# Performance work log

Hardware: AMD Instinct MI355X
Metric: run time of the kernel (lower is better)

Reference implementation:

```python
import jax, jax.numpy as jnp
import numpy as np

OMEGA = 0.3        # self.omega
NU = 0.2           # self.nu
LAMBDA_DECAY = 0.1 # lambda_decay
MU_INIT = 0.25     # nn.Parameter init
EPS_DENOM = 1e-8
EPS_SQRT = 1e-24   # safe sqrt (avoids nan grad at exactly-zero distance)


def setup_inputs() -> dict:
    key = jax.random.key(0)
    k1, k2, k3, k4 = jax.random.split(key, 4)
    T, D = 4096, 896  # seq_len, Qwen2.5-0.5B hidden size
    return {
        "hidden_states": jax.random.normal(k1, (T, D), dtype=jnp.float32),
        "m_t": jax.random.uniform(k2, (T,), dtype=jnp.float32),
        "c_t": jax.random.uniform(k3, (T,), dtype=jnp.float32),
        "d_t": jax.random.uniform(k4, (T,), dtype=jnp.float32),
        "mu": jnp.asarray(MU_INIT, dtype=jnp.float32),
    }


def _semantic_drift(hidden_states, m_t, c_t, d_t, mu):
    T, D = hidden_states.shape
    # F.normalize(h, p=2, dim=1): x / max(||x||, eps)
    norms = jnp.linalg.norm(hidden_states, axis=1, keepdims=True)
    h = hidden_states / jnp.maximum(norms, 1e-12)          # [T, D]

    # Causal decayed-softmax anchor: alpha[t, s] over s <= t
    sim = jnp.einsum("td,sd->ts", h, h)                    # [T, T], h(s)^T h(t) at row t
    idx = jnp.arange(T)
    tds = (idx[:, None] - idx[None, :]).astype(jnp.float32)  # t - s
    causal = tds >= 0.0
    sqrt_d = jnp.sqrt(jnp.asarray(D, jnp.float32))
    denom = sqrt_d * jnp.exp(LAMBDA_DECAY * tds) + EPS_DENOM
    logits = jnp.where(causal, sim / denom, -jnp.inf)
    alpha = jax.nn.softmax(logits, axis=1)                 # [T, T]
    g = jnp.einsum("ts,sd->td", alpha, h)                  # h_global(t), [T, D]

    # dist(h(t), h_global(t)) — normalize_hidden=True, so plain euclidean norm
    dist = jnp.sqrt(jnp.maximum(jnp.sum((h - g) ** 2, axis=1), EPS_SQRT))  # [T]

    # dist_max(t) = max_{s<=t} ||h(s) - h_global(t)|| (torch loop starts max at 0)
    hn2 = jnp.sum(h * h, axis=1)                           # [T]
    gn2 = jnp.sum(g * g, axis=1)                           # [T]
    cross = jnp.einsum("td,sd->ts", g, h)                  # g(t)·h(s)
    d2 = jnp.maximum(hn2[None, :] - 2.0 * cross + gn2[:, None], EPS_SQRT)
    dmat = jnp.sqrt(d2)                                    # [T, T], dist(h(s), g(t))
    dist_max = jnp.max(jnp.where(causal, dmat, 0.0), axis=1)
    dist_max = jnp.where(dist_max < 1e-6, 1.0, dist_max)

    dist_ratio = dist / (dist_max + EPS_DENOM)
    stability = 1.0 - OMEGA * c_t + NU * d_t
    xi = 1.0 - mu * m_t
    return jnp.clip(dist_ratio * stability * xi, 0.0, 1.0)  # [T]


def reference(hidden_states, m_t, c_t, d_t, mu):
    return _semantic_drift(hidden_states, m_t, c_t, d_t, mu)
```

## Files before the change

### kernel.cpp

```cpp
#include <hip/hip_runtime.h>
#include <math.h>


#define T_ 4096
#define D_ 896
#define TP (T_ + 64)
#define PSTR 900

typedef float f32x4 __attribute__((ext_vector_type(4)));
typedef unsigned short u16x8 __attribute__((ext_vector_type(8)));
typedef __bf16 bf16x8 __attribute__((ext_vector_type(8)));

union V16 { uint4 u; u16x8 v; };

__device__ __forceinline__ u16x8 ld16(const unsigned short* p) {
  V16 x; x.u = *(const uint4*)p; return x.v;
}
__device__ __forceinline__ void st16(unsigned short* p, u16x8 v) {
  V16 x; x.v = v; *(uint4*)p = x.u;
}
__device__ __forceinline__ unsigned short f2bf(float f) {
  unsigned int u = __float_as_uint(f);
  u += 0x7FFFu + ((u >> 16) & 1u);
  return (unsigned short)(u >> 16);
}
__device__ __forceinline__ float bf2f(unsigned short b) {
  return __uint_as_float(((unsigned int)b) << 16);
}
__device__ __forceinline__ f32x4 mfma16(u16x8 a, u16x8 b, f32x4 c) {
  return __builtin_amdgcn_mfma_f32_16x16x32_bf16(
      __builtin_bit_cast(bf16x8, a), __builtin_bit_cast(bf16x8, b), c, 0, 0, 0);
}

typedef __attribute__((address_space(1))) const void glob_cv;
typedef __attribute__((address_space(3))) void lds_v;
__device__ __forceinline__ void gload16(const void* g, void* l) {
  __builtin_amdgcn_global_load_lds((glob_cv*)g, (lds_v*)l, 16, 0, 0);
}

__device__ __forceinline__ void stage32(const unsigned short* __restrict__ g0,
                                        int stride, unsigned short* lds0, int tid) {
  #pragma unroll
  for (int it = 0; it < 2; ++it) {
    const int e = it * 256 + tid;
    const int row = e >> 3, pg = e & 7;
    const int gg = pg ^ (row & 7);
    gload16(g0 + (size_t)row * stride + gg * 8, lds0 + e * 8);
  }
}

__device__ __forceinline__ void tri2_decode(int b, int& ti, int& sj) {
  int p = (int)((sqrtf(4.0f * (float)b + 1.0f) - 1.0f) * 0.5f);
  while ((p + 1) * (p + 2) <= b) ++p;
  while (p * (p + 1) > b) --p;
  const int r = b - p * (p + 1);
  if (r >= p + 1) { ti = 2 * p + 1; sj = r - (p + 1); }
  else            { ti = 2 * p;     sj = r; }
}

__global__ __launch_bounds__(256, 2) void k_prep2(const float* __restrict__ x,
    float* __restrict__ invnorm, unsigned short* __restrict__ hb,
    unsigned short* __restrict__ hbTp, float* __restrict__ Sseg,
    float* __restrict__ zero3) {
  __shared__ unsigned short Ts[16 * PSTR];
  const int b = (int)blockIdx.x;
  const int t0 = b * 16;
  const int tid = (int)threadIdx.x, wv = tid >> 6, lane = tid & 63;

  if (b < 48) zero3[b * 256 + tid] = 0.f;

  float4 v[4][4];
  #pragma unroll
  for (int rr = 0; rr < 4; ++rr) {
    const int t = t0 + wv * 4 + rr;
    #pragma unroll
    for (int k = 0; k < 4; ++k) {
      const int c4 = lane + 64 * k;
      if (k < 3 || lane < 32)
        v[rr][k] = *(const float4*)(x + (size_t)t * D_ + c4 * 4);
    }
  }
  #pragma unroll
  for (int rr = 0; rr < 4; ++rr) {
    const int row = wv * 4 + rr;
    const int t = t0 + row;
    float s = 0.f;
    #pragma unroll
    for (int k = 0; k < 4; ++k)
      if (k < 3 || lane < 32)
        s += v[rr][k].x * v[rr][k].x + v[rr][k].y * v[rr][k].y +
             v[rr][k].z * v[rr][k].z + v[rr][k].w * v[rr][k].w;
    #pragma unroll
    for (int off = 32; off > 0; off >>= 1) s += __shfl_down(s, off, 64);
    const float iv = 1.0f / fmaxf(sqrtf(__shfl(s, 0, 64)), 1e-12f);
    if (lane == 0) invnorm[t] = iv;
    #pragma unroll
    for (int k = 0; k < 4; ++k) {
      const int c4 = lane + 64 * k;
      if (k < 3 || lane < 32) {
        const ushort4 o = make_ushort4(f2bf(v[rr][k].x * iv), f2bf(v[rr][k].y * iv),
                                       f2bf(v[rr][k].z * iv), f2bf(v[rr][k].w * iv));
        *(ushort4*)(hb + (size_t)t * D_ + c4 * 4) = o;
        *(ushort4*)(&Ts[row * PSTR + c4 * 4]) = o;
      }
    }
  }
  __syncthreads();

  for (int c = tid; c < D_; c += 256) {
    float segsum = 0.f;
    #pragma unroll
    for (int q = 0; q < 4; ++q) {
      float gs = 0.f;
      #pragma unroll
      for (int r = 0; r < 4; ++r)
        gs += bf2f(Ts[(q * 4 + r) * PSTR + c]);
      segsum += gs;
    }
    Sseg[(size_t)b * D_ + c] = segsum;
  }

  #pragma unroll 2
  for (int it = 0; it < 14; ++it) {
    const int e = it * 256 + tid;
    const int d = e >> 2, q = e & 3;
    const ushort4 o = make_ushort4(Ts[(q * 4 + 0) * PSTR + d],
                                   Ts[(q * 4 + 1) * PSTR + d],
                                   Ts[(q * 4 + 2) * PSTR + d],
                                   Ts[(q * 4 + 3) * PSTR + d]);
    *(ushort4*)(hbTp + (size_t)d * TP + 32 + t0 + q * 4) = o;
  }
  if (b == 0) {
    for (int e = tid; e < D_ * 8; e += 256) {
      const int d = e >> 3, cc = (e & 7) * 4;
      *(ushort4*)(hbTp + (size_t)d * TP + cc) = make_ushort4(0, 0, 0, 0);
    }
  }
}

__global__ __launch_bounds__(256) void k_bandw(const unsigned short* __restrict__ hb,
    const float* __restrict__ Sseg, float* __restrict__ Eseg,
    unsigned short* __restrict__ wband, float* __restrict__ invLb) {
  const int b = (int)blockIdx.x;
  const int t0 = b * 16;
  const int tid = (int)threadIdx.x;
  const int wv = tid >> 6, lane = tid & 63;
  const int tcol = lane & 15, quad = lane >> 4;
  __shared__ float sims[16][52];
  if (wv < 3) {
    const int s_base = t0 - 32 + wv * 16;
    if (s_base + 15 >= 0) {
      const int srow = max(s_base + tcol, 0);
      f32x4 acc = {};
      const unsigned short* arow = hb + (size_t)srow * D_ + quad * 8;
      const unsigned short* brow = hb + (size_t)(t0 + tcol) * D_ + quad * 8;
      #pragma unroll 1
      for (int c4 = 0; c4 < 4; ++c4) {
        u16x8 av[7], bv[7];
        #pragma unroll
        for (int i = 0; i < 7; ++i) {
          av[i] = ld16(arow + (c4 * 7 + i) * 32);
          bv[i] = ld16(brow + (c4 * 7 + i) * 32);
        }
        #pragma unroll
        for (int i = 0; i < 7; ++i) acc = mfma16(av[i], bv[i], acc);
      }
      #pragma unroll
      for (int r = 0; r < 4; ++r)
        sims[tcol][wv * 16 + quad * 4 + r] = acc[r];
    }
  } else if (b < 224) {
    #pragma unroll 1
    for (int cc = 0; cc < 4; ++cc) {
      const int c = b * 4 + cc;
      float v0 = Sseg[(size_t)lane * D_ + c];
      float v1 = Sseg[(size_t)(64 + lane) * D_ + c];
      float v2 = Sseg[(size_t)(128 + lane) * D_ + c];
      float v3 = Sseg[(size_t)(192 + lane) * D_ + c];
      const float o0 = v0, o1 = v1, o2 = v2, o3 = v3;
      #pragma unroll
      for (int off = 1; off < 64; off <<= 1) {
        const float n0 = __shfl_up(v0, off, 64);
        const float n1 = __shfl_up(v1, off, 64);
        const float n2 = __shfl_up(v2, off, 64);
        const float n3 = __shfl_up(v3, off, 64);
        if (lane >= off) { v0 += n0; v1 += n1; v2 += n2; v3 += n3; }
      }
      const float tot0 = __shfl(v0, 63, 64);
      const float tot1 = __shfl(v1, 63, 64);
      const float tot2 = __shfl(v2, 63, 64);
      Eseg[(size_t)lane * D_ + c] = v0 - o0;
      Eseg[(size_t)(64 + lane) * D_ + c] = v1 - o1 + tot0;
      Eseg[(size_t)(128 + lane) * D_ + c] = v2 - o2 + (tot0 + tot1);
      Eseg[(size_t)(192 + lane) * D_ + c] = v3 - o3 + (tot0 + tot1 + tot2);
    }
  }
  __syncthreads();
  if (wv == 0) {
    u16x8 af0, af1;
    float lsum = 0.f;
    #pragma unroll
    for (int j = 0; j < 8; ++j) {
      {
        const int k = quad * 8 + j;
        const int dt = tcol + 32 - k;
        const int s = t0 - 32 + k;
        unsigned short wb = 0;
        if (dt < 32 && s >= 0)
          wb = f2bf(__expf(sims[tcol][k] * (__expf(-0.1f * (float)dt) * 0.033407657f)));
        af0[j] = wb;
        lsum += bf2f(wb);
      }
      {
        const int k = 32 + quad * 8 + j;
        const int dt = tcol + 32 - k;
        unsigned short wb = 0;
        if (dt >= 0)
          wb = f2bf(__expf(sims[tcol][k] * (__expf(-0.1f * (float)dt) * 0.033407657f)));
        af1[j] = wb;
        lsum += bf2f(wb);
      }
    }
    lsum += __shfl_xor(lsum, 16, 64);
    lsum += __shfl_xor(lsum, 32, 64);
    st16(wband + (size_t)(t0 + tcol) * 64 + quad * 8, af0);
    st16(wband + (size_t)(t0 + tcol) * 64 + 32 + quad * 8, af1);
    if (lane < 16) {
      const int t = t0 + lane;
      invLb[t] = 1.0f / (lsum + ((t >= 32) ? (float)(t - 31) : 0.f));
    }
  }
}

__global__ __launch_bounds__(256) void k_bandg(const unsigned short* __restrict__ hbTp,
    const unsigned short* __restrict__ wband, const float* __restrict__ invLb,
    const float* __restrict__ Eseg, const float* __restrict__ x,
    const float* __restrict__ invnorm, unsigned short* __restrict__ gb,
    float* __restrict__ gn2, float* __restrict__ dist2) {
  const int t0 = (int)blockIdx.x * 16;
  const int by = (int)blockIdx.y;
  const int tid = (int)threadIdx.x;
  const int wv = tid >> 6, lane = tid & 63;
  const int tcol = lane & 15, quad = lane >> 4;
  const u16x8 af0 = ld16(wband + (size_t)(t0 + tcol) * 64 + quad * 8);
  const u16x8 af1 = ld16(wband + (size_t)(t0 + tcol) * 64 + 32 + quad * 8);
  const int sg = (t0 >> 4) - 2;
  float invLr[4], inrr[4];
  #pragma unroll
  for (int r = 0; r < 4; ++r) {
    const int tt = t0 + quad * 4 + r;
    invLr[r] = invLb[tt];
    inrr[r]  = invnorm[tt];
  }
  float sgl[4] = {0.f, 0.f, 0.f, 0.f}, sdl[4] = {0.f, 0.f, 0.f, 0.f};
  for (int i = wv; i < 7; i += 4) {
    const int d = (by * 7 + i) * 16 + tcol;
    const unsigned short* brow = hbTp + (size_t)d * TP + t0 + quad * 8;
    const u16x8 b0 = ld16(brow);
    const u16x8 b1 = ld16(brow + 32);
    f32x4 C = {};
    C = mfma16(af0, b0, C);
    C = mfma16(af1, b1, C);
    float pr[4] = {0.f, 0.f, 0.f, 0.f};
    if (t0 >= 32) {
      const unsigned short* prow = hbTp + (size_t)d * TP + t0;
      const uint4 w0 = *(const uint4*)prow;
      const uint4 w1 = *(const uint4*)(prow + 8);
      const unsigned int wz[8] = {w0.x, w0.y, w0.z, w0.w, w1.x, w1.y, w1.z, w1.w};
      float run = Eseg[(size_t)sg * D_ + d];
      #pragma unroll
      for (int jj = 0; jj < 16; ++jj) {
        const unsigned int uu = wz[jj >> 1];
        const unsigned short hh =
            (jj & 1) ? (unsigned short)(uu >> 16) : (unsigned short)(uu & 0xffffu);
        run += bf2f(hh);
        if ((jj >> 2) == quad) pr[jj & 3] = run;
      }
    }
    #pragma unroll
    for (int r = 0; r < 4; ++r) {
      const int tt = t0 + quad * 4 + r;
      float gacc = C[r];
      if (tt >= 32) gacc += pr[r];
      const float g = gacc * invLr[r];
      gb[(size_t)tt * D_ + d] = f2bf(g);
      const float e = x[(size_t)tt * D_ + d] * inrr[r] - g;
      sgl[r] += g * g;
      sdl[r] += e * e;
    }
  }
  #pragma unroll
  for (int r = 0; r < 4; ++r) {
    float sg2 = sgl[r], sd = sdl[r];
    sg2 += __shfl_xor(sg2, 1, 64); sg2 += __shfl_xor(sg2, 2, 64);
    sg2 += __shfl_xor(sg2, 4, 64); sg2 += __shfl_xor(sg2, 8, 64);
    sd += __shfl_xor(sd, 1, 64); sd += __shfl_xor(sd, 2, 64);
    sd += __shfl_xor(sd, 4, 64); sd += __shfl_xor(sd, 8, 64);
    if (tcol == 0) {
      atomicAdd(&gn2[t0 + quad * 4 + r], sg2);
      atomicAdd(&dist2[t0 + quad * 4 + r], sd);
    }
  }
}

__global__ __launch_bounds__(256, 5) void k_gemm3(const unsigned short* __restrict__ gb,
    const unsigned short* __restrict__ hb, const float* __restrict__ gn2,
    unsigned int* __restrict__ dmaxu) {
  const int bswz = ((int)blockIdx.x & 7) * 132 + ((int)blockIdx.x >> 3);
  int ti, sj;
  tri2_decode(bswz, ti, sj);
  const int t0 = ti * 64, s0 = sj * 128;
  __shared__ unsigned short As[64 * 64];
  __shared__ unsigned short Bs[128 * 64];
  __shared__ unsigned int dmx[64];
  const int tid = (int)threadIdx.x;
  const int lane = tid & 63, wv = tid >> 6;
  const int tcol = lane & 15, quad = lane >> 4;
  if (tid < 64) dmx[tid] = 0u;
  f32x4 acc[4][2] = {};

  for (int kc = 0; kc < 14; ++kc) {
    __syncthreads();
    stage32(gb + (size_t)t0 * D_ + kc * 64, D_, As, tid);
    stage32(hb + (size_t)s0 * D_ + kc * 64, D_, Bs, tid);
    stage32(hb + (size_t)(s0 + 64) * D_ + kc * 64, D_, Bs + 64 * 64, tid);
    __syncthreads();
    #pragma unroll
    for (int ks = 0; ks < 2; ++ks) {
      const int go = ((ks * 4 + quad) ^ (tcol & 7)) * 8;
      u16x8 bf[2], af[4];
      #pragma unroll
      for (int ni = 0; ni < 2; ++ni)
        bf[ni] = ld16(&Bs[(wv * 32 + ni * 16 + tcol) * 64 + go]);
      #pragma unroll
      for (int mi = 0; mi < 4; ++mi)
        af[mi] = ld16(&As[(mi * 16 + tcol) * 64 + go]);
      #pragma unroll
      for (int mi = 0; mi < 4; ++mi)
        #pragma unroll
        for (int ni = 0; ni < 2; ++ni)
          acc[mi][ni] = mfma16(af[mi], bf[ni], acc[mi][ni]);
    }
  }

  #pragma unroll
  for (int mi = 0; mi < 4; ++mi) {
    #pragma unroll
    for (int r = 0; r < 4; ++r) {
      const int t = t0 + mi * 16 + quad * 4 + r;
      const float gn = gn2[t];
      float m2 = 0.f;
      #pragma unroll
      for (int ni = 0; ni < 2; ++ni) {
        const int s = s0 + wv * 32 + ni * 16 + tcol;
        if (t >= s)
          m2 = fmaxf(m2, fmaxf(1.0f - 2.0f * acc[mi][ni][r] + gn, 1e-24f));
      }
      m2 = fmaxf(m2, __shfl_xor(m2, 1, 64));
      m2 = fmaxf(m2, __shfl_xor(m2, 2, 64));
      m2 = fmaxf(m2, __shfl_xor(m2, 4, 64));
      m2 = fmaxf(m2, __shfl_xor(m2, 8, 64));
      if (tcol == 0 && m2 > 0.f)
        atomicMax(&dmx[mi * 16 + quad * 4 + r], __float_as_uint(m2));
    }
  }
  __syncthreads();
  if (tid < 64) {
    const unsigned int v = dmx[tid];
    if (v) atomicMax(&dmaxu[t0 + tid], v);
  }
}

__global__ __launch_bounds__(256) void k_final(const float* __restrict__ m_t,
    const float* __restrict__ c_t, const float* __restrict__ d_t,
    const float* __restrict__ mu, const float* __restrict__ dist2,
    const unsigned int* __restrict__ dmaxu, float* __restrict__ out) {
  const int t = (int)blockIdx.x * 256 + (int)threadIdx.x;
  if (t >= T_) return;
  float ratio;
  if (t == 0) {
    ratio = 0.f;
  } else {
    float dmax = sqrtf(__uint_as_float(dmaxu[t]));
    if (dmax < 1e-6f) dmax = 1.0f;
    ratio = sqrtf(fmaxf(dist2[t], 1e-24f)) / (dmax + 1e-8f);
  }
  const float stab = 1.0f - 0.3f * c_t[t] + 0.2f * d_t[t];
  const float xi = 1.0f - mu[0] * m_t[t];
  out[t] = fminf(fmaxf(ratio * stab * xi, 0.f), 1.f);
}

extern "C" void kernel_launch(void* const* d_in, const int* in_sizes, int n_in,
                              void* d_out, int out_size, void* d_ws, size_t ws_size,
                              hipStream_t stream) {
  const float* x   = (const float*)d_in[0];
  const float* m_t = (const float*)d_in[1];
  const float* c_t = (const float*)d_in[2];
  const float* d_t = (const float*)d_in[3];
  const float* mu  = (const float*)d_in[4];
  float* out = (float*)d_out;

  float* ws = (float*)d_ws;
  float* invnorm = ws;
  unsigned int* dmaxu = (unsigned int*)(ws + (size_t)T_);
  float* gn2     = ws + 2 * (size_t)T_;
  float* dist2   = ws + 3 * (size_t)T_;
  float* invLb   = ws + 4 * (size_t)T_;
  float* Sseg    = ws + 5 * (size_t)T_;
  float* Eseg    = Sseg + 256 * (size_t)D_;
  float* Pold    = Eseg + 256 * (size_t)D_;
  unsigned short* hb    = (unsigned short*)(Pold + (size_t)T_ * D_);
  unsigned short* hbTp  = hb + (size_t)T_ * D_;
  unsigned short* gb    = hbTp + (size_t)D_ * TP;
  unsigned short* wband = gb + (size_t)T_ * D_;

  float* zero3 = ws + (size_t)T_;

  k_prep2<<<T_ / 16, 256, 0, stream>>>(x, invnorm, hb, hbTp, Sseg, zero3);
  k_bandw<<<T_ / 16, 256, 0, stream>>>(hb, Sseg, Eseg, wband, invLb);
  k_bandg<<<dim3(T_ / 16, 8), 256, 0, stream>>>(hbTp, wband, invLb, Eseg, x, invnorm,
                                                gb, gn2, dist2);
  k_gemm3<<<1056, 256, 0, stream>>>(gb, hb, gn2, dmaxu);
  k_final<<<(T_ + 255) / 256, 256, 0, stream>>>(m_t, c_t, d_t, mu, dist2, dmaxu, out);
}
```

Measured before the change: 135.6 us.

## Fuse final epilogue into gemm3 via last-block-per-row-tile counter

Removes the separate k_final launch. Each gemm3 block bumps a per-row-tile counter, and the last block to finish a tile computes the outputs for its 64 rows, reading dmax through an atomic to get coherence. The zeroing of the hbTp padding is also spread across 28 blocks instead of being done serially by block 0. This trades one kernel launch for extra atomics and fences, plus a counter that must be reset in prep.

```diff
diff --git a/kernel.cpp b/kernel.cpp
--- a/kernel.cpp
+++ b/kernel.cpp
@@ -61,13 +61,14 @@
 __global__ __launch_bounds__(256, 2) void k_prep2(const float* __restrict__ x,
     float* __restrict__ invnorm, unsigned short* __restrict__ hb,
     unsigned short* __restrict__ hbTp, float* __restrict__ Sseg,
-    float* __restrict__ zero3) {
+    float* __restrict__ zero3, unsigned int* __restrict__ cnt) {
   __shared__ unsigned short Ts[16 * PSTR];
   const int b = (int)blockIdx.x;
   const int t0 = b * 16;
   const int tid = (int)threadIdx.x, wv = tid >> 6, lane = tid & 63;
 
   if (b < 48) zero3[b * 256 + tid] = 0.f;
+  else if (b == 48 && tid < 64) cnt[tid] = 0u;
 
   float4 v[4][4];
   #pragma unroll
@@ -130,11 +131,9 @@
                                    Ts[(q * 4 + 3) * PSTR + d]);
     *(ushort4*)(hbTp + (size_t)d * TP + 32 + t0 + q * 4) = o;
   }
-  if (b == 0) {
-    for (int e = tid; e < D_ * 8; e += 256) {
-      const int d = e >> 3, cc = (e & 7) * 4;
-      *(ushort4*)(hbTp + (size_t)d * TP + cc) = make_ushort4(0, 0, 0, 0);
-    }
+  if (b < 28) {
+    const int d = b * 32 + (tid >> 3), cc = (tid & 7) * 4;
+    *(ushort4*)(hbTp + (size_t)d * TP + cc) = make_ushort4(0, 0, 0, 0);
   }
 }
 
@@ -305,7 +304,10 @@
 
 __global__ __launch_bounds__(256, 5) void k_gemm3(const unsigned short* __restrict__ gb,
     const unsigned short* __restrict__ hb, const float* __restrict__ gn2,
-    unsigned int* __restrict__ dmaxu) {
+    unsigned int* __restrict__ dmaxu, unsigned int* __restrict__ cnt,
+    const float* __restrict__ dist2, const float* __restrict__ m_t,
+    const float* __restrict__ c_t, const float* __restrict__ d_t,
+    const float* __restrict__ mu, float* __restrict__ out) {
   const int bswz = ((int)blockIdx.x & 7) * 132 + ((int)blockIdx.x >> 3);
   int ti, sj;
   tri2_decode(bswz, ti, sj);
@@ -313,6 +315,7 @@
   __shared__ unsigned short As[64 * 64];
   __shared__ unsigned short Bs[128 * 64];
   __shared__ unsigned int dmx[64];
+  __shared__ int lastflag;
   const int tid = (int)threadIdx.x;
   const int lane = tid & 63, wv = tid >> 6;
   const int tcol = lane & 15, quad = lane >> 4;
@@ -368,26 +371,30 @@
   if (tid < 64) {
     const unsigned int v = dmx[tid];
     if (v) atomicMax(&dmaxu[t0 + tid], v);
-  }
-}
-
-__global__ __launch_bounds__(256) void k_final(const float* __restrict__ m_t,
-    const float* __restrict__ c_t, const float* __restrict__ d_t,
-    const float* __restrict__ mu, const float* __restrict__ dist2,
-    const unsigned int* __restrict__ dmaxu, float* __restrict__ out) {
-  const int t = (int)blockIdx.x * 256 + (int)threadIdx.x;
-  if (t >= T_) return;
-  float ratio;
-  if (t == 0) {
-    ratio = 0.f;
-  } else {
-    float dmax = sqrtf(__uint_as_float(dmaxu[t]));
-    if (dmax < 1e-6f) dmax = 1.0f;
-    ratio = sqrtf(fmaxf(dist2[t], 1e-24f)) / (dmax + 1e-8f);
-  }
-  const float stab = 1.0f - 0.3f * c_t[t] + 0.2f * d_t[t];
-  const float xi = 1.0f - mu[0] * m_t[t];
-  out[t] = fminf(fmaxf(ratio * stab * xi, 0.f), 1.f);
+    __threadfence();
+  }
+  __syncthreads();
+  if (tid == 0) {
+    const unsigned int need = (unsigned int)(ti / 2 + 1);
+    const unsigned int pos = atomicAdd(&cnt[ti], 1u);
+    lastflag = (pos == need - 1u) ? 1 : 0;
+  }
+  __syncthreads();
+  if (lastflag && tid < 64) {
+    const int t = t0 + tid;
+    float ratio;
+    if (t == 0) {
+      ratio = 0.f;
+    } else {
+      const unsigned int du = atomicMax(&dmaxu[t], 0u);
+      float dmax = sqrtf(__uint_as_float(du));
+      if (dmax < 1e-6f) dmax = 1.0f;
+      ratio = sqrtf(fmaxf(dist2[t], 1e-24f)) / (dmax + 1e-8f);
+    }
+    const float stab = 1.0f - 0.3f * c_t[t] + 0.2f * d_t[t];
+    const float xi = 1.0f - mu[0] * m_t[t];
+    out[t] = fminf(fmaxf(ratio * stab * xi, 0.f), 1.f);
+  }
 }
 
 extern "C" void kernel_launch(void* const* d_in, const int* in_sizes, int n_in,
@@ -408,7 +415,8 @@
   float* invLb   = ws + 4 * (size_t)T_;
   float* Sseg    = ws + 5 * (size_t)T_;
   float* Eseg    = Sseg + 256 * (size_t)D_;
-  float* Pold    = Eseg + 256 * (size_t)D_;
+  unsigned int* cnt = (unsigned int*)(Eseg + 256 * (size_t)D_);
+  float* Pold    = Eseg + 256 * (size_t)D_ + 256;
   unsigned short* hb    = (unsigned short*)(Pold + (size_t)T_ * D_);
   unsigned short* hbTp  = hb + (size_t)T_ * D_;
   unsigned short* gb    = hbTp + (size_t)D_ * TP;
@@ -416,10 +424,10 @@
 
   float* zero3 = ws + (size_t)T_;
 
-  k_prep2<<<T_ / 16, 256, 0, stream>>>(x, invnorm, hb, hbTp, Sseg, zero3);
+  k_prep2<<<T_ / 16, 256, 0, stream>>>(x, invnorm, hb, hbTp, Sseg, zero3, cnt);
   k_bandw<<<T_ / 16, 256, 0, stream>>>(hb, Sseg, Eseg, wband, invLb);
   k_bandg<<<dim3(T_ / 16, 8), 256, 0, stream>>>(hbTp, wband, invLb, Eseg, x, invnorm,
                                                 gb, gn2, dist2);
-  k_gemm3<<<1056, 256, 0, stream>>>(gb, hb, gn2, dmaxu);
-  k_final<<<(T_ + 255) / 256, 256, 0, stream>>>(m_t, c_t, d_t, mu, dist2, dmaxu, out);
-}
+  k_gemm3<<<1056, 256, 0, stream>>>(gb, hb, gn2, dmaxu, cnt, dist2,
+                                    m_t, c_t, d_t, mu, out);
+}
```

Result: slower. 144.1 us (+6.3%).
